# Kernel tuning notes

Hardware: AMD Instinct MI355X
Metric: run time of the kernel (lower is better)

## Reference

```python
import jax, jax.numpy as jnp
import numpy as np

N = 50000      # nodes
E = 800000     # edges
D = 128        # in_channels
H = 128        # hidden_channels
G = 64         # graphs in batch
OUT = 10       # out_channels
L = 6          # gcn layers (hardcoded in module)
EPS = 1e-5     # batchnorm eps


def setup_inputs() -> dict:
    key = jax.random.key(0)
    ks = jax.random.split(key, 8)
    s = 1.0 / np.sqrt(H)
    return {
        "x": jax.random.normal(ks[0], (N, D), jnp.float32),
        "edge_index": jax.random.randint(ks[1], (2, E), 0, N),
        "batch": jnp.sort(jax.random.randint(ks[2], (N,), 0, G)),
        "conv_W": jax.random.normal(ks[3], (L, D, H), jnp.float32) * s,
        "conv_b": jnp.zeros((L, H), jnp.float32),
        "bn_gamma": jnp.ones((L - 1, H), jnp.float32),
        "bn_beta": jnp.zeros((L - 1, H), jnp.float32),
        "head_W1": jax.random.normal(ks[4], (H, H), jnp.float32) * s,
        "head_b1": jnp.zeros((H,), jnp.float32),
        "head_bn_gamma": jnp.ones((H,), jnp.float32),
        "head_bn_beta": jnp.zeros((H,), jnp.float32),
        "head_W2": jax.random.normal(ks[5], (H, H), jnp.float32) * s,
        "head_b2": jnp.zeros((H,), jnp.float32),
        "head_W3": jax.random.normal(ks[6], (H, OUT), jnp.float32) * s,
        "head_b3": jnp.zeros((OUT,), jnp.float32),
    }


def _batchnorm(h, gamma, beta):
    # track_running_stats=False -> always batch statistics, biased variance
    mu = h.mean(axis=0)
    var = jnp.mean((h - mu) ** 2, axis=0)
    return (h - mu) * jax.lax.rsqrt(var + EPS) * gamma + beta


def reference(x, edge_index, batch, conv_W, conv_b, bn_gamma, bn_beta,
              head_W1, head_b1, head_bn_gamma, head_bn_beta,
              head_W2, head_b2, head_W3, head_b3):
    src, dst = edge_index[0], edge_index[1]
    # GCN symmetric norm with self-loops: deg = in-degree + 1
    deg = jnp.zeros((N,), x.dtype).at[dst].add(1.0) + 1.0
    dinv = jax.lax.rsqrt(deg)                 # deg^{-1/2}
    enorm = (dinv[src] * dinv[dst])[:, None]  # [E,1] edge weights
    self_w = (dinv * dinv)[:, None]           # [N,1] self-loop weight = 1/deg

    h = x
    for i in range(L):
        h = h @ conv_W[i]                                     # [N,H]
        agg = jnp.zeros_like(h).at[dst].add(h[src] * enorm)   # scatter-add
        h = agg + h * self_w + conv_b[i]
        if i < L - 1:
            h = jax.nn.relu(_batchnorm(h, bn_gamma[i], bn_beta[i]))
            # dropout(p=0.1) -> identity in eval

    # global_mean_pool over graphs
    counts = jnp.zeros((G,), h.dtype).at[batch].add(1.0)
    pooled = jnp.zeros((G, H), h.dtype).at[batch].add(h)
    pooled = pooled / jnp.clip(counts, 1.0)[:, None]

    # prediction head: Linear -> BN -> ReLU -> (Dropout) -> Linear -> ReLU -> Linear
    z = pooled @ head_W1 + head_b1
    z = jax.nn.relu(_batchnorm(z, head_bn_gamma, head_bn_beta))
    z = jax.nn.relu(z @ head_W2 + head_b2)
    return z @ head_W3 + head_b3
```

## Files before the change

### kernel.cpp

```cpp
#include <hip/hip_runtime.h>

#define N 50000
#define E 800000
#define H 128
#define G 64
#define OUTC 10
#define L 6
#define EPS 1e-5f

typedef unsigned short ushort_t;
typedef __attribute__((ext_vector_type(8))) short short8;
typedef __attribute__((ext_vector_type(8))) unsigned short ushort8;
typedef __attribute__((ext_vector_type(4))) float floatx4;

__device__ __forceinline__ void atomAddF(float* p, float v) {
  unsafeAtomicAdd(p, v);
}

__device__ __forceinline__ unsigned short f2bf(float f) {
  unsigned u = __float_as_uint(f);
  unsigned r = (u + 0x7FFF + ((u >> 16) & 1)) >> 16;
  return (unsigned short)r;
}
__device__ __forceinline__ float bf2f(unsigned short b) {
  return __uint_as_float(((unsigned)b) << 16);
}

__global__ void zero_kernel(int* __restrict__ p, int n) {
  int i = blockIdx.x * blockDim.x + threadIdx.x;
  if (i < n) p[i] = 0;
}

__global__ void deg_count_kernel(const int* __restrict__ dst, int* __restrict__ deg) {
  int e = blockIdx.x * blockDim.x + threadIdx.x;
  if (e < E) atomicAdd(&deg[dst[e]], 1);
}

__global__ void dinv_kernel(const int* __restrict__ deg, float* __restrict__ dinv) {
  int n = blockIdx.x * blockDim.x + threadIdx.x;
  if (n < N) dinv[n] = rsqrtf((float)(deg[n] + 1));
}

__global__ void prep_kernel(const float* __restrict__ x, const float* __restrict__ convW,
                            ushort_t* __restrict__ xb, ushort_t* __restrict__ WT) {
  int i = blockIdx.x * 256 + threadIdx.x;
  if (i < N * H) {
    xb[i] = f2bf(x[i]);
  } else {
    int j = i - N * H;
    if (j < L * H * H) {
      int l = j >> 14, r = j & 16383;
      int n = r >> 7, k = r & 127;
      WT[j] = f2bf(convW[l * 16384 + k * 128 + n]);
    }
  }
}

#define SCAN_B ((N + 255) / 256)

__global__ __launch_bounds__(256) void scanA_kernel(const int* __restrict__ deg,
                                                    int* __restrict__ blocksum) {
  __shared__ int red[256];
  int i = blockIdx.x * 256 + threadIdx.x;
  int v = (i < N) ? deg[i] : 0;
  red[threadIdx.x] = v;
  __syncthreads();
  for (int off = 128; off > 0; off >>= 1) {
    if (threadIdx.x < off) red[threadIdx.x] += red[threadIdx.x + off];
    __syncthreads();
  }
  if (threadIdx.x == 0) blocksum[blockIdx.x] = red[0];
}

__global__ __launch_bounds__(256) void scanB_kernel(int* __restrict__ blocksum) {
  __shared__ int sh[256];
  int t = threadIdx.x;
  sh[t] = (t < SCAN_B) ? blocksum[t] : 0;
  __syncthreads();
  for (int off = 1; off < 256; off <<= 1) {
    int v = (t >= off) ? sh[t - off] : 0;
    __syncthreads();
    sh[t] += v;
    __syncthreads();
  }
  if (t < SCAN_B) blocksum[t] = (t == 0) ? 0 : sh[t - 1];
}

__global__ __launch_bounds__(256) void scanC_kernel(const int* __restrict__ deg,
                                                    const int* __restrict__ blocksum,
                                                    int* __restrict__ rowptr) {
  __shared__ int sh[256];
  int i = blockIdx.x * 256 + threadIdx.x;
  int t = threadIdx.x;
  int d = (i < N) ? deg[i] : 0;
  sh[t] = d;
  __syncthreads();
  for (int off = 1; off < 256; off <<= 1) {
    int v = (t >= off) ? sh[t - off] : 0;
    __syncthreads();
    sh[t] += v;
    __syncthreads();
  }
  if (i < N) rowptr[i] = blocksum[blockIdx.x] + sh[t] - d;
  if (i == 0) rowptr[N] = E;
}

__global__ void csr_fill_kernel(const int* __restrict__ src, const int* __restrict__ dst,
                                const int* __restrict__ rowptr,
                                int* __restrict__ cursor, int* __restrict__ csr) {
  int e = blockIdx.x * blockDim.x + threadIdx.x;
  if (e < E) {
    int d = dst[e];
    int pos = rowptr[d] + atomicAdd(&cursor[d], 1);
    csr[pos] = src[e];
  }
}

__global__ void cnt_kernel(const int* __restrict__ batch, float* __restrict__ cnt) {
  __shared__ int lb[G + 1];
  int t = threadIdx.x;
  if (t <= G) {
    int lo = 0, hi = N;
    while (lo < hi) { int m = (lo + hi) >> 1; if (batch[m] < t) lo = m + 1; else hi = m; }
    lb[t] = lo;
  }
  __syncthreads();
  if (t < G) cnt[t] = (float)(lb[t + 1] - lb[t]);
}

__global__ __launch_bounds__(256) void gemm_mfma_kernel(
    const ushort_t* __restrict__ Ab, const ushort_t* __restrict__ WT,
    const float* __restrict__ dinv, ushort_t* __restrict__ hWs,
    const float* __restrict__ bnsums, const float* __restrict__ gamma,
    const float* __restrict__ beta)
{
  const int tid = threadIdx.x;
  const int wave = tid >> 6, lane = tid & 63;
  const int quad = lane >> 4, m = lane & 15;
  const int row0 = blockIdx.x * 64 + wave * 16;
  const int arow = min(row0 + m, N - 1);
  const float invN = 1.0f / (float)N;

  short8 afrag[4];
#pragma unroll
  for (int kc = 0; kc < 4; ++kc) {
    ushort8 raw = *(const ushort8*)&Ab[arow * H + kc * 32 + quad * 8];
    if (bnsums) {
      const int k0 = kc * 32 + quad * 8;
#pragma unroll
      for (int j = 0; j < 8; ++j) {
        float s = bnsums[k0 + j], q = bnsums[128 + k0 + j];
        float mu = s * invN;
        float var = q * invN - mu * mu;
        float rs = rsqrtf(var + EPS);
        float sc = gamma[k0 + j] * rs;
        float sh = beta[k0 + j] - mu * sc;
        raw[j] = f2bf(fmaxf(bf2f(raw[j]) * sc + sh, 0.f));
      }
    }
    short8 a;
#pragma unroll
    for (int j = 0; j < 8; ++j) a[j] = (short)raw[j];
    afrag[kc] = a;
  }

  float dv[4];
#pragma unroll
  for (int i = 0; i < 4; ++i) {
    int r = row0 + quad * 4 + i;
    dv[i] = (r < N) ? dinv[r] : 0.f;
  }

  const short* WTs = (const short*)WT;
#pragma unroll
  for (int nt = 0; nt < 8; ++nt) {
    floatx4 acc = {0.f, 0.f, 0.f, 0.f};
#pragma unroll
    for (int kc = 0; kc < 4; ++kc) {
      short8 bfrag = *(const short8*)&WTs[(nt * 16 + m) * H + kc * 32 + quad * 8];
      acc = __builtin_amdgcn_mfma_f32_16x16x32_bf16(afrag[kc], bfrag, acc, 0, 0, 0);
    }
    int col = nt * 16 + m;
#pragma unroll
    for (int i = 0; i < 4; ++i) {
      int r = row0 + quad * 4 + i;
      if (r < N) hWs[r * H + col] = f2bf(acc[i] * dv[i]);
    }
  }
}

__global__ __launch_bounds__(256) void gather_kernel(
    const ushort_t* __restrict__ hWs, const int* __restrict__ csr,
    const int* __restrict__ rowptr, const float* __restrict__ dinv,
    const float* __restrict__ bias, ushort_t* __restrict__ aggb)
{
  int t = blockIdx.x * 256 + threadIdx.x;
  int n = t >> 4, c8 = (t & 15) * 8;

  ushort8 us = *(const ushort8*)&hWs[n * H + c8];
  float acc[8];
#pragma unroll
  for (int j = 0; j < 8; ++j) acc[j] = bf2f(us[j]);

  int e = rowptr[n], end = rowptr[n + 1];
  for (; e + 3 < end; e += 4) {
    int s0 = csr[e], s1 = csr[e + 1], s2 = csr[e + 2], s3 = csr[e + 3];
    ushort8 u0 = *(const ushort8*)&hWs[s0 * H + c8];
    ushort8 u1 = *(const ushort8*)&hWs[s1 * H + c8];
    ushort8 u2 = *(const ushort8*)&hWs[s2 * H + c8];
    ushort8 u3 = *(const ushort8*)&hWs[s3 * H + c8];
#pragma unroll
    for (int j = 0; j < 8; ++j)
      acc[j] += (bf2f(u0[j]) + bf2f(u1[j])) + (bf2f(u2[j]) + bf2f(u3[j]));
  }
  for (; e < end; ++e) {
    int s0 = csr[e];
    ushort8 u0 = *(const ushort8*)&hWs[s0 * H + c8];
#pragma unroll
    for (int j = 0; j < 8; ++j) acc[j] += bf2f(u0[j]);
  }

  float dn = dinv[n];
  float4 b0 = *(const float4*)&bias[c8];
  float4 b1 = *(const float4*)&bias[c8 + 4];
  float bb[8] = {b0.x, b0.y, b0.z, b0.w, b1.x, b1.y, b1.z, b1.w};
  ushort8 o;
#pragma unroll
  for (int j = 0; j < 8; ++j) o[j] = f2bf(acc[j] * dn + bb[j]);
  *(ushort8*)&aggb[n * H + c8] = o;
}

__global__ __launch_bounds__(256) void bn_stats_kernel(
    const ushort_t* __restrict__ a, float* __restrict__ sums)
{
  __shared__ float red[256];
  int tid = threadIdx.x;
  int c = tid & 127, half = tid >> 7;
  int r0 = blockIdx.x * 128;
  float s = 0.f, q = 0.f;
  for (int i = 0; i < 64; ++i) {
    int r = r0 + i * 2 + half;
    if (r < N) { float v = bf2f(a[r * H + c]); s += v; q += v * v; }
  }
  red[tid] = s; __syncthreads();
  float s2 = (half == 0) ? s + red[tid + 128] : 0.f;
  __syncthreads();
  red[tid] = q; __syncthreads();
  if (half == 0) {
    float q2 = q + red[tid + 128];
    atomAddF(&sums[c], s2);
    atomAddF(&sums[128 + c], q2);
  }
}

__global__ __launch_bounds__(256) void pool_kernel(
    const ushort_t* __restrict__ h, const int* __restrict__ batch,
    float* __restrict__ pooled )
{
  int r0 = blockIdx.x * 128;
  int rend = min(r0 + 128, N);
  int c = threadIdx.x & 127, half = threadIdx.x >> 7;
  float acc = 0.f;
  int curg = -1;
  for (int r = r0 + half; r < rend; r += 2) {
    int g = batch[r];
    if (g != curg) {
      if (curg >= 0) atomAddF(&pooled[curg * H + c], acc);
      acc = 0.f; curg = g;
    }
    acc += bf2f(h[r * H + c]);
  }
  if (curg >= 0) atomAddF(&pooled[curg * H + c], acc);
}

__global__ void head1_kernel(const float* __restrict__ pooled, const float* __restrict__ cnt,
                             const float* __restrict__ W1, const float* __restrict__ b1,
                             float* __restrict__ z1)
{
  int t = blockIdx.x * 256 + threadIdx.x;
  int g = t >> 7, c = t & 127;
  float s = 0.f;
  for (int k = 0; k < H; ++k) s += pooled[g * H + k] * W1[k * H + c];
  z1[t] = s / fmaxf(cnt[g], 1.0f) + b1[c];
}

__global__ void head_bn_kernel(float* __restrict__ z1,
                               const float* __restrict__ gamma, const float* __restrict__ beta)
{
  int c = threadIdx.x;
  float s = 0.f, q = 0.f;
  for (int g = 0; g < G; ++g) { float v = z1[g * H + c]; s += v; q += v * v; }
  float mu = s / (float)G;
  float var = q / (float)G - mu * mu;
  float rs = rsqrtf(var + EPS);
  float ga = gamma[c], be = beta[c];
  for (int g = 0; g < G; ++g) {
    float v = z1[g * H + c];
    z1[g * H + c] = fmaxf((v - mu) * rs * ga + be, 0.f);
  }
}

__global__ void head2_kernel(const float* __restrict__ z1, const float* __restrict__ W2,
                             const float* __restrict__ b2, float* __restrict__ z2)
{
  int t = blockIdx.x * 256 + threadIdx.x;
  int g = t >> 7, c = t & 127;
  float s = b2[c];
  for (int k = 0; k < H; ++k) s += z1[g * H + k] * W2[k * H + c];
  z2[t] = fmaxf(s, 0.f);
}

__global__ void head3_kernel(const float* __restrict__ z2, const float* __restrict__ W3,
                             const float* __restrict__ b3, float* __restrict__ out)
{
  int t = blockIdx.x * 256 + threadIdx.x;
  if (t < G * OUTC) {
    int g = t / OUTC, o = t % OUTC;
    float s = b3[o];
    for (int k = 0; k < H; ++k) s += z2[g * H + k] * W3[k * OUTC + o];
    out[t] = s;
  }
}

extern "C" void kernel_launch(void* const* d_in, const int* in_sizes, int n_in,
                              void* d_out, int out_size, void* d_ws, size_t ws_size,
                              hipStream_t stream) {
  const float* x     = (const float*)d_in[0];
  const int*   ei    = (const int*)d_in[1];
  const int*   srcp  = ei;
  const int*   dstp  = ei + E;
  const int*   batch = (const int*)d_in[2];
  const float* convW = (const float*)d_in[3];
  const float* convb = (const float*)d_in[4];
  const float* bng   = (const float*)d_in[5];
  const float* bnb   = (const float*)d_in[6];
  const float* W1    = (const float*)d_in[7];
  const float* b1    = (const float*)d_in[8];
  const float* hg    = (const float*)d_in[9];
  const float* hb    = (const float*)d_in[10];
  const float* W2    = (const float*)d_in[11];
  const float* b2    = (const float*)d_in[12];
  const float* W3    = (const float*)d_in[13];
  const float* b3    = (const float*)d_in[14];
  float* out = (float*)d_out;

  const size_t NH2 = (size_t)N * H / 2;
  float*    ws     = (float*)d_ws;
  ushort_t* xb     = (ushort_t*)ws;
  ushort_t* aggb   = (ushort_t*)(ws + NH2);
  ushort_t* hWs    = (ushort_t*)(ws + 2 * NH2);
  ushort_t* WT     = (ushort_t*)(ws + 3 * NH2);
  float*    dinv   = ws + 3 * NH2 + (L * H * H / 2);
  int*      rowptr = (int*)(dinv + N);
  int*      csr    = rowptr + N + 1;
  int*      deg    = csr + E;
  int*      cursor = deg + N;
  float*    bnsums = (float*)(cursor + N);
  float*    pooled = bnsums + (L - 1) * 256;
  float*    cnt    = pooled + G * H;
  float*    z1     = cnt + G;
  float*    z2     = z1 + G * H;
  int*      bsum   = (int*)(z2 + G * H);

  const int zero_words = N + N + (L - 1) * 256 + G * H;
  zero_kernel<<<(zero_words + 255) / 256, 256, 0, stream>>>(deg, zero_words);
  deg_count_kernel<<<(E + 255) / 256, 256, 0, stream>>>(dstp, deg);
  dinv_kernel<<<(N + 255) / 256, 256, 0, stream>>>(deg, dinv);
  scanA_kernel<<<SCAN_B, 256, 0, stream>>>(deg, bsum);
  scanB_kernel<<<1, 256, 0, stream>>>(bsum);
  scanC_kernel<<<SCAN_B, 256, 0, stream>>>(deg, bsum, rowptr);
  csr_fill_kernel<<<(E + 255) / 256, 256, 0, stream>>>(srcp, dstp, rowptr, cursor, csr);
  cnt_kernel<<<1, 128, 0, stream>>>(batch, cnt);
  prep_kernel<<<(N * H + L * H * H + 255) / 256, 256, 0, stream>>>(x, convW, xb, WT);

  for (int l = 0; l < L; ++l) {
    const ushort_t* Ab = (l == 0) ? xb : aggb;
    const float* bs = (l == 0) ? nullptr : bnsums + (l - 1) * 256;
    const float* ga = (l == 0) ? nullptr : bng + (size_t)(l - 1) * H;
    const float* be = (l == 0) ? nullptr : bnb + (size_t)(l - 1) * H;
    gemm_mfma_kernel<<<(N + 63) / 64, 256, 0, stream>>>(
        Ab, WT + (size_t)l * H * H, dinv, hWs, bs, ga, be);
    gather_kernel<<<N * 16 / 256, 256, 0, stream>>>(
        hWs, csr, rowptr, dinv, convb + (size_t)l * H, aggb);
    if (l < L - 1)
      bn_stats_kernel<<<(N + 127) / 128, 256, 0, stream>>>(aggb, bnsums + l * 256);
  }

  pool_kernel<<<(N + 127) / 128, 256, 0, stream>>>(aggb, batch, pooled);
  head1_kernel<<<32, 256, 0, stream>>>(pooled, cnt, W1, b1, z1);
  head_bn_kernel<<<1, 128, 0, stream>>>(z1, hg, hb);
  head2_kernel<<<32, 256, 0, stream>>>(z1, W2, b2, z2);
  head3_kernel<<<3, 256, 0, stream>>>(z2, W3, b3, out);
}
```

Baseline: 714.1 us.

## Switch activations to fp32 with split-bf16 MFMA GEMM for accuracy

Activations (hWs, agg) move from bf16 to fp32 storage. The GEMM now splits A and W into hi/lo bf16 parts and issues three MFMAs per step to approximate fp32 precision. The gather reads float4 per lane with 8-way unrolling. A few setup kernels are also merged: dinv is folded into scanA, scanB into scanC, the zero kernel becomes hipMemsetAsync, and x is no longer pre-converted. This mainly buys accuracy, at the cost of twice the gather/BN memory traffic and three times the MFMA work.

```diff
diff --git a/kernel.cpp b/kernel.cpp
--- a/kernel.cpp
+++ b/kernel.cpp
@@ -10,7 +10,6 @@
 
 typedef unsigned short ushort_t;
 typedef __attribute__((ext_vector_type(8))) short short8;
-typedef __attribute__((ext_vector_type(8))) unsigned short ushort8;
 typedef __attribute__((ext_vector_type(4))) float floatx4;
 
 __device__ __forceinline__ void atomAddF(float* p, float v) {
@@ -26,43 +25,33 @@
   return __uint_as_float(((unsigned)b) << 16);
 }
 
-__global__ void zero_kernel(int* __restrict__ p, int n) {
-  int i = blockIdx.x * blockDim.x + threadIdx.x;
-  if (i < n) p[i] = 0;
-}
-
 __global__ void deg_count_kernel(const int* __restrict__ dst, int* __restrict__ deg) {
   int e = blockIdx.x * blockDim.x + threadIdx.x;
   if (e < E) atomicAdd(&deg[dst[e]], 1);
 }
 
-__global__ void dinv_kernel(const int* __restrict__ deg, float* __restrict__ dinv) {
-  int n = blockIdx.x * blockDim.x + threadIdx.x;
-  if (n < N) dinv[n] = rsqrtf((float)(deg[n] + 1));
-}
-
-__global__ void prep_kernel(const float* __restrict__ x, const float* __restrict__ convW,
-                            ushort_t* __restrict__ xb, ushort_t* __restrict__ WT) {
-  int i = blockIdx.x * 256 + threadIdx.x;
-  if (i < N * H) {
-    xb[i] = f2bf(x[i]);
-  } else {
-    int j = i - N * H;
-    if (j < L * H * H) {
-      int l = j >> 14, r = j & 16383;
-      int n = r >> 7, k = r & 127;
-      WT[j] = f2bf(convW[l * 16384 + k * 128 + n]);
-    }
+__global__ void prep_kernel(const float* __restrict__ convW,
+                            ushort_t* __restrict__ WThi, ushort_t* __restrict__ WTlo) {
+  int j = blockIdx.x * 256 + threadIdx.x;
+  if (j < L * H * H) {
+    int l = j >> 14, r = j & 16383;
+    int n = r >> 7, k = r & 127;
+    float w = convW[l * 16384 + k * 128 + n];
+    unsigned short hi = f2bf(w);
+    WThi[j] = hi;
+    WTlo[j] = f2bf(w - bf2f(hi));
   }
 }
 
 #define SCAN_B ((N + 255) / 256)
 
 __global__ __launch_bounds__(256) void scanA_kernel(const int* __restrict__ deg,
-                                                    int* __restrict__ blocksum) {
+                                                    int* __restrict__ blocksum,
+                                                    float* __restrict__ dinv) {
   __shared__ int red[256];
   int i = blockIdx.x * 256 + threadIdx.x;
   int v = (i < N) ? deg[i] : 0;
+  if (i < N) dinv[i] = rsqrtf((float)(v + 1));
   red[threadIdx.x] = v;
   __syncthreads();
   for (int off = 128; off > 0; off >>= 1) {
@@ -72,10 +61,22 @@
   if (threadIdx.x == 0) blocksum[blockIdx.x] = red[0];
 }
 
-__global__ __launch_bounds__(256) void scanB_kernel(int* __restrict__ blocksum) {
+__global__ __launch_bounds__(256) void scanC_kernel(const int* __restrict__ deg,
+                                                    const int* __restrict__ blocksum,
+                                                    int* __restrict__ rowptr) {
+  __shared__ int pre[256];
   __shared__ int sh[256];
-  int t = threadIdx.x;
-  sh[t] = (t < SCAN_B) ? blocksum[t] : 0;
+  const int bid = blockIdx.x, t = threadIdx.x;
+  pre[t] = (t < bid) ? blocksum[t] : 0;
+  __syncthreads();
+  for (int off = 128; off > 0; off >>= 1) {
+    if (t < off) pre[t] += pre[t + off];
+    __syncthreads();
+  }
+  int base = pre[0];
+  int i = bid * 256 + t;
+  int d = (i < N) ? deg[i] : 0;
+  sh[t] = d;
   __syncthreads();
   for (int off = 1; off < 256; off <<= 1) {
     int v = (t >= off) ? sh[t - off] : 0;
@@ -83,25 +84,7 @@
     sh[t] += v;
     __syncthreads();
   }
-  if (t < SCAN_B) blocksum[t] = (t == 0) ? 0 : sh[t - 1];
-}
-
-__global__ __launch_bounds__(256) void scanC_kernel(const int* __restrict__ deg,
-                                                    const int* __restrict__ blocksum,
-                                                    int* __restrict__ rowptr) {
-  __shared__ int sh[256];
-  int i = blockIdx.x * 256 + threadIdx.x;
-  int t = threadIdx.x;
-  int d = (i < N) ? deg[i] : 0;
-  sh[t] = d;
-  __syncthreads();
-  for (int off = 1; off < 256; off <<= 1) {
-    int v = (t >= off) ? sh[t - off] : 0;
-    __syncthreads();
-    sh[t] += v;
-    __syncthreads();
-  }
-  if (i < N) rowptr[i] = blocksum[blockIdx.x] + sh[t] - d;
+  if (i < N) rowptr[i] = base + sh[t] - d;
   if (i == 0) rowptr[N] = E;
 }
 
@@ -129,8 +112,9 @@
 }
 
 __global__ __launch_bounds__(256) void gemm_mfma_kernel(
-    const ushort_t* __restrict__ Ab, const ushort_t* __restrict__ WT,
-    const float* __restrict__ dinv, ushort_t* __restrict__ hWs,
+    const float* __restrict__ A,
+    const ushort_t* __restrict__ WThi, const ushort_t* __restrict__ WTlo,
+    const float* __restrict__ dinv, float* __restrict__ hWs,
     const float* __restrict__ bnsums, const float* __restrict__ gamma,
     const float* __restrict__ beta)
 {
@@ -141,12 +125,14 @@
   const int arow = min(row0 + m, N - 1);
   const float invN = 1.0f / (float)N;
 
-  short8 afrag[4];
+  short8 ahi[4], alo[4];
 #pragma unroll
   for (int kc = 0; kc < 4; ++kc) {
-    ushort8 raw = *(const ushort8*)&Ab[arow * H + kc * 32 + quad * 8];
+    const int k0 = kc * 32 + quad * 8;
+    float4 f0 = *(const float4*)&A[arow * H + k0];
+    float4 f1 = *(const float4*)&A[arow * H + k0 + 4];
+    float vals[8] = {f0.x, f0.y, f0.z, f0.w, f1.x, f1.y, f1.z, f1.w};
     if (bnsums) {
-      const int k0 = kc * 32 + quad * 8;
 #pragma unroll
       for (int j = 0; j < 8; ++j) {
         float s = bnsums[k0 + j], q = bnsums[128 + k0 + j];
@@ -155,13 +141,18 @@
         float rs = rsqrtf(var + EPS);
         float sc = gamma[k0 + j] * rs;
         float sh = beta[k0 + j] - mu * sc;
-        raw[j] = f2bf(fmaxf(bf2f(raw[j]) * sc + sh, 0.f));
+        vals[j] = fmaxf(vals[j] * sc + sh, 0.f);
       }
     }
-    short8 a;
-#pragma unroll
-    for (int j = 0; j < 8; ++j) a[j] = (short)raw[j];
-    afrag[kc] = a;
+    short8 h, l;
+#pragma unroll
+    for (int j = 0; j < 8; ++j) {
+      unsigned short hb = f2bf(vals[j]);
+      h[j] = (short)hb;
+      l[j] = (short)f2bf(vals[j] - bf2f(hb));
+    }
+    ahi[kc] = h;
+    alo[kc] = l;
   }
 
   float dv[4];
@@ -171,67 +162,79 @@
     dv[i] = (r < N) ? dinv[r] : 0.f;
   }
 
-  const short* WTs = (const short*)WT;
+  const short* WH = (const short*)WThi;
+  const short* WL = (const short*)WTlo;
 #pragma unroll
   for (int nt = 0; nt < 8; ++nt) {
     floatx4 acc = {0.f, 0.f, 0.f, 0.f};
 #pragma unroll
     for (int kc = 0; kc < 4; ++kc) {
-      short8 bfrag = *(const short8*)&WTs[(nt * 16 + m) * H + kc * 32 + quad * 8];
-      acc = __builtin_amdgcn_mfma_f32_16x16x32_bf16(afrag[kc], bfrag, acc, 0, 0, 0);
+      const int boff = (nt * 16 + m) * H + kc * 32 + quad * 8;
+      short8 bhi = *(const short8*)&WH[boff];
+      short8 blo = *(const short8*)&WL[boff];
+      acc = __builtin_amdgcn_mfma_f32_16x16x32_bf16(ahi[kc], bhi, acc, 0, 0, 0);
+      acc = __builtin_amdgcn_mfma_f32_16x16x32_bf16(alo[kc], bhi, acc, 0, 0, 0);
+      acc = __builtin_amdgcn_mfma_f32_16x16x32_bf16(ahi[kc], blo, acc, 0, 0, 0);
     }
     int col = nt * 16 + m;
 #pragma unroll
     for (int i = 0; i < 4; ++i) {
       int r = row0 + quad * 4 + i;
-      if (r < N) hWs[r * H + col] = f2bf(acc[i] * dv[i]);
+      if (r < N) hWs[r * H + col] = acc[i] * dv[i];
     }
   }
 }
 
 __global__ __launch_bounds__(256) void gather_kernel(
-    const ushort_t* __restrict__ hWs, const int* __restrict__ csr,
+    const float* __restrict__ hWs, const int* __restrict__ csr,
     const int* __restrict__ rowptr, const float* __restrict__ dinv,
-    const float* __restrict__ bias, ushort_t* __restrict__ aggb)
+    const float* __restrict__ bias, float* __restrict__ agg)
 {
   int t = blockIdx.x * 256 + threadIdx.x;
-  int n = t >> 4, c8 = (t & 15) * 8;
-
-  ushort8 us = *(const ushort8*)&hWs[n * H + c8];
-  float acc[8];
-#pragma unroll
-  for (int j = 0; j < 8; ++j) acc[j] = bf2f(us[j]);
+  int n = t >> 5, c4 = (t & 31) * 4;
+
+  float4 self = *(const float4*)&hWs[n * H + c4];
+  float ax = self.x, ay = self.y, az = self.z, aw = self.w;
 
   int e = rowptr[n], end = rowptr[n + 1];
-  for (; e + 3 < end; e += 4) {
+  for (; e + 7 < end; e += 8) {
     int s0 = csr[e], s1 = csr[e + 1], s2 = csr[e + 2], s3 = csr[e + 3];
-    ushort8 u0 = *(const ushort8*)&hWs[s0 * H + c8];
-    ushort8 u1 = *(const ushort8*)&hWs[s1 * H + c8];
-    ushort8 u2 = *(const ushort8*)&hWs[s2 * H + c8];
-    ushort8 u3 = *(const ushort8*)&hWs[s3 * H + c8];
-#pragma unroll
-    for (int j = 0; j < 8; ++j)
-      acc[j] += (bf2f(u0[j]) + bf2f(u1[j])) + (bf2f(u2[j]) + bf2f(u3[j]));
-  }
-  for (; e < end; ++e) {
+    int s4 = csr[e + 4], s5 = csr[e + 5], s6 = csr[e + 6], s7 = csr[e + 7];
+    float4 u0 = *(const float4*)&hWs[s0 * H + c4];
+    float4 u1 = *(const float4*)&hWs[s1 * H + c4];
+    float4 u2 = *(const float4*)&hWs[s2 * H + c4];
+    float4 u3 = *(const float4*)&hWs[s3 * H + c4];
+    float4 u4 = *(const float4*)&hWs[s4 * H + c4];
+    float4 u5 = *(const float4*)&hWs[s5 * H + c4];
+    float4 u6 = *(const float4*)&hWs[s6 * H + c4];
+    float4 u7 = *(const float4*)&hWs[s7 * H + c4];
+    ax += ((u0.x + u1.x) + (u2.x + u3.x)) + ((u4.x + u5.x) + (u6.x + u7.x));
+    ay += ((u0.y + u1.y) + (u2.y + u3.y)) + ((u4.y + u5.y) + (u6.y + u7.y));
+    az += ((u0.z + u1.z) + (u2.z + u3.z)) + ((u4.z + u5.z) + (u6.z + u7.z));
+    aw += ((u0.w + u1.w) + (u2.w + u3.w)) + ((u4.w + u5.w) + (u6.w + u7.w));
+  }
+  for (; e + 1 < end; e += 2) {
+    int s0 = csr[e], s1 = csr[e + 1];
+    float4 u0 = *(const float4*)&hWs[s0 * H + c4];
+    float4 u1 = *(const float4*)&hWs[s1 * H + c4];
+    ax += u0.x + u1.x; ay += u0.y + u1.y;
+    az += u0.z + u1.z; aw += u0.w + u1.w;
+  }
+  if (e < end) {
     int s0 = csr[e];
-    ushort8 u0 = *(const ushort8*)&hWs[s0 * H + c8];
-#pragma unroll
-    for (int j = 0; j < 8; ++j) acc[j] += bf2f(u0[j]);
+    float4 u0 = *(const float4*)&hWs[s0 * H + c4];
+    ax += u0.x; ay += u0.y; az += u0.z; aw += u0.w;
   }
 
   float dn = dinv[n];
-  float4 b0 = *(const float4*)&bias[c8];
-  float4 b1 = *(const float4*)&bias[c8 + 4];
-  float bb[8] = {b0.x, b0.y, b0.z, b0.w, b1.x, b1.y, b1.z, b1.w};
-  ushort8 o;
-#pragma unroll
-  for (int j = 0; j < 8; ++j) o[j] = f2bf(acc[j] * dn + bb[j]);
-  *(ushort8*)&aggb[n * H + c8] = o;
+  float4 bv = *(const float4*)&bias[c4];
+  float4 o = make_float4(ax * dn + bv.x, ay * dn + bv.y,
+                         az * dn + bv.z, aw * dn + bv.w);
+  *(float4*)&agg[n * H + c4] = o;
 }
 
 __global__ __launch_bounds__(256) void bn_stats_kernel(
-    const ushort_t* __restrict__ a, float* __restrict__ sums)
+    const float* __restrict__ a, float* __restrict__ sums)
 {
   __shared__ float red[256];
   int tid = threadIdx.x;
@@ -240,7 +243,7 @@
   float s = 0.f, q = 0.f;
   for (int i = 0; i < 64; ++i) {
     int r = r0 + i * 2 + half;
-    if (r < N) { float v = bf2f(a[r * H + c]); s += v; q += v * v; }
+    if (r < N) { float v = a[r * H + c]; s += v; q += v * v; }
   }
   red[tid] = s; __syncthreads();
   float s2 = (half == 0) ? s + red[tid + 128] : 0.f;
@@ -254,7 +257,7 @@
 }
 
 __global__ __launch_bounds__(256) void pool_kernel(
-    const ushort_t* __restrict__ h, const int* __restrict__ batch,
+    const float* __restrict__ h, const int* __restrict__ batch,
     float* __restrict__ pooled )
 {
   int r0 = blockIdx.x * 128;
@@ -268,7 +271,7 @@
       if (curg >= 0) atomAddF(&pooled[curg * H + c], acc);
       acc = 0.f; curg = g;
     }
-    acc += bf2f(h[r * H + c]);
+    acc += h[r * H + c];
   }
   if (curg >= 0) atomAddF(&pooled[curg * H + c], acc);
 }
@@ -344,13 +347,12 @@
   const float* b3    = (const float*)d_in[14];
   float* out = (float*)d_out;
 
-  const size_t NH2 = (size_t)N * H / 2;
   float*    ws     = (float*)d_ws;
-  ushort_t* xb     = (ushort_t*)ws;
-  ushort_t* aggb   = (ushort_t*)(ws + NH2);
-  ushort_t* hWs    = (ushort_t*)(ws + 2 * NH2);
-  ushort_t* WT     = (ushort_t*)(ws + 3 * NH2);
-  float*    dinv   = ws + 3 * NH2 + (L * H * H / 2);
+  float*    agg    = ws;
+  float*    hWs    = agg + (size_t)N * H;
+  ushort_t* WThi   = (ushort_t*)(hWs + (size_t)N * H);
+  ushort_t* WTlo   = WThi + (size_t)L * H * H;
+  float*    dinv   = (float*)(WTlo + (size_t)L * H * H);
   int*      rowptr = (int*)(dinv + N);
   int*      csr    = rowptr + N + 1;
   int*      deg    = csr + E;
@@ -362,31 +364,29 @@
   float*    z2     = z1 + G * H;
   int*      bsum   = (int*)(z2 + G * H);
 
-  const int zero_words = N + N + (L - 1) * 256 + G * H;
-  zero_kernel<<<(zero_words + 255) / 256, 256, 0, stream>>>(deg, zero_words);
+  const size_t zero_bytes = (size_t)(N + N + (L - 1) * 256 + G * H) * 4;
+  hipMemsetAsync(deg, 0, zero_bytes, stream);
   deg_count_kernel<<<(E + 255) / 256, 256, 0, stream>>>(dstp, deg);
-  dinv_kernel<<<(N + 255) / 256, 256, 0, stream>>>(deg, dinv);
-  scanA_kernel<<<SCAN_B, 256, 0, stream>>>(deg, bsum);
-  scanB_kernel<<<1, 256, 0, stream>>>(bsum);
+  scanA_kernel<<<SCAN_B, 256, 0, stream>>>(deg, bsum, dinv);
   scanC_kernel<<<SCAN_B, 256, 0, stream>>>(deg, bsum, rowptr);
   csr_fill_kernel<<<(E + 255) / 256, 256, 0, stream>>>(srcp, dstp, rowptr, cursor, csr);
+  prep_kernel<<<(L * H * H + 255) / 256, 256, 0, stream>>>(convW, WThi, WTlo);
   cnt_kernel<<<1, 128, 0, stream>>>(batch, cnt);
-  prep_kernel<<<(N * H + L * H * H + 255) / 256, 256, 0, stream>>>(x, convW, xb, WT);
 
   for (int l = 0; l < L; ++l) {
-    const ushort_t* Ab = (l == 0) ? xb : aggb;
+    const float* A  = (l == 0) ? x : agg;
     const float* bs = (l == 0) ? nullptr : bnsums + (l - 1) * 256;
     const float* ga = (l == 0) ? nullptr : bng + (size_t)(l - 1) * H;
     const float* be = (l == 0) ? nullptr : bnb + (size_t)(l - 1) * H;
     gemm_mfma_kernel<<<(N + 63) / 64, 256, 0, stream>>>(
-        Ab, WT + (size_t)l * H * H, dinv, hWs, bs, ga, be);
-    gather_kernel<<<N * 16 / 256, 256, 0, stream>>>(
-        hWs, csr, rowptr, dinv, convb + (size_t)l * H, aggb);
+        A, WThi + (size_t)l * H * H, WTlo + (size_t)l * H * H, dinv, hWs, bs, ga, be);
+    gather_kernel<<<N * 32 / 256, 256, 0, stream>>>(
+        hWs, csr, rowptr, dinv, convb + (size_t)l * H, agg);
     if (l < L - 1)
-      bn_stats_kernel<<<(N + 127) / 128, 256, 0, stream>>>(aggb, bnsums + l * 256);
-  }
-
-  pool_kernel<<<(N + 127) / 128, 256, 0, stream>>>(aggb, batch, pooled);
+      bn_stats_kernel<<<(N + 127) / 128, 256, 0, stream>>>(agg, bnsums + l * 256);
+  }
+
+  pool_kernel<<<(N + 127) / 128, 256, 0, stream>>>(agg, batch, pooled);
   head1_kernel<<<32, 256, 0, stream>>>(pooled, cnt, W1, b1, z1);
   head_bn_kernel<<<1, 128, 0, stream>>>(z1, hg, hb);
   head2_kernel<<<32, 256, 0, stream>>>(z1, W2, b2, z2);
```

Result: slower. 965.9 us (+35.3%).
